# Optimization experiments

Measured on AMD Instinct MI355X. Metric: run time of the kernel, lower is better.

## Reference

```python
import jax, jax.numpy as jnp
import numpy as np
from jax import lax

B, T, S_ENC = 64, 32, 64
E, H, V = 1024, 1024, 32000


def setup_inputs() -> dict:
    key = jax.random.key(0)
    ks = jax.random.split(key, 12)
    s = 0.02
    return {
        "inputs": jax.random.randint(ks[0], (B, T), 0, V),
        "encoder_outputs": jax.random.normal(ks[1], (B, S_ENC, 2 * H), jnp.float32),
        "h0": jax.random.normal(ks[2], (B, H), jnp.float32) * 0.1,
        "c0": jax.random.normal(ks[3], (B, H), jnp.float32) * 0.1,
        "emb": jax.random.normal(ks[4], (V, E), jnp.float32) * s,
        "W_ih": jax.random.normal(ks[5], (4 * H, E), jnp.float32) * s,
        "W_hh": jax.random.normal(ks[6], (4 * H, H), jnp.float32) * s,
        "b_ih": jnp.zeros((4 * H,), jnp.float32),
        "b_hh": jnp.zeros((4 * H,), jnp.float32),
        "attn_W": jax.random.normal(ks[7], (2 * H, H), jnp.float32) * s,  # Linear(H -> 2H, no bias)
        "comb_W": jax.random.normal(ks[8], (H, 3 * H), jnp.float32) * s,  # Linear(3H -> H)
        "comb_b": jnp.zeros((H,), jnp.float32),
        "out_W": jax.random.normal(ks[9], (V, H), jnp.float32) * s,       # Linear(H -> V)
        "out_b": jnp.zeros((V,), jnp.float32),
    }


def _decode(inputs, encoder_outputs, h0, c0, emb, W_ih, W_hh, b_ih, b_hh,
            attn_W, comb_W, comb_b, out_W, out_b):
    x = emb[inputs]                      # [B, T, E]
    bias = b_ih + b_hh

    def step(carry, x_t):
        h, c = carry                     # [B, H] each
        gates = x_t @ W_ih.T + h @ W_hh.T + bias    # [B, 4H]
        i, f, g, o = jnp.split(gates, 4, axis=-1)   # PyTorch LSTM gate order
        i, f, o = jax.nn.sigmoid(i), jax.nn.sigmoid(f), jax.nn.sigmoid(o)
        c = f * c + i * jnp.tanh(g)
        h = o * jnp.tanh(c)
        # Luong-style attention (faithful to source, incl. softmax over dim=1 of size 1)
        ah = h @ attn_W.T                                        # [B, 2H]
        scores = jnp.einsum('bd,bsd->bs', ah, encoder_outputs)[:, None, :]  # [B,1,S]
        w = jax.nn.softmax(scores, axis=1)                       # size-1 axis -> all ones
        ctx = jnp.einsum('bqs,bsd->bqd', w, encoder_outputs)[:, 0]          # [B, 2H]
        merged = jnp.concatenate([h, ctx], axis=-1)              # [B, 3H]
        out = jnp.tanh(merged @ comb_W.T + comb_b)               # [B, H]
        return (h, c), out

    (h, c), outs = lax.scan(step, (h0, c0), x.transpose(1, 0, 2))
    outputs = outs.transpose(1, 0, 2)                            # [B, T, H]
    logits = outputs @ out_W.T + out_b                           # [B, T, V]
    return logits, h, c


def reference(inputs, encoder_outputs, h0, c0, emb, W_ih, W_hh, b_ih, b_hh,
              attn_W, comb_W, comb_b, out_W, out_b):
    return _decode(inputs, encoder_outputs, h0, c0, emb, W_ih, W_hh, b_ih, b_hh,
                   attn_W, comb_W, comb_b, out_W, out_b)
```

## Files before the change

kernel.cpp:

```cpp
#include <hip/hip_runtime.h>
#include <hip/hip_bf16.h>


typedef unsigned short u16;
typedef unsigned int u32;
typedef short s8v __attribute__((ext_vector_type(8)));
typedef float f4v __attribute__((ext_vector_type(4)));

__device__ __forceinline__ u16 f2bf(float f) {
  unsigned x = __float_as_uint(f);
  return (u16)((x + 0x7fffu + ((x >> 16) & 1u)) >> 16);
}
__device__ __forceinline__ float bf2f(u16 u) {
  return __uint_as_float(((unsigned)u) << 16);
}

__device__ __forceinline__ void gl_lds16(const void* g, void* l) {
  __builtin_amdgcn_global_load_lds(
      (const __attribute__((address_space(1))) u32*)g,
      (__attribute__((address_space(3))) u32*)l, 16, 0, 0);
}

__device__ __forceinline__ int xcd_swz(int bid, int nb) {
  int q8 = nb >> 3, r8 = nb & 7;
  int xcd = bid & 7, idx = bid >> 3;
  return (xcd < r8 ? xcd * (q8 + 1) : r8 * (q8 + 1) + (xcd - r8) * q8) + idx;
}

template <int EPI>
__global__ __launch_bounds__(512, 1) void gemm_q(
    const u16* __restrict__ A, const u16* __restrict__ Bm,
    const float* __restrict__ bias, void* __restrict__ Cp,
    int K, int ldc, int gridM) {
  __shared__ __align__(16) u16 LDS[2 * 32768];

  int swz = xcd_swz((int)blockIdx.x, (int)gridDim.x);
  int mt = swz % gridM, nt = swz / gridM;
  long bm = (long)mt * 256, bn = (long)nt * 256;

  int tid = threadIdx.x;
  int w = tid >> 6, l = tid & 63;
  int wm = w & 1, wn = w >> 1;
  int lr = l & 15, lg = l >> 4;

  int nt_k = K >> 6;

  auto stage = [&](int s, int kt_idx) {
    int kt = kt_idx << 6;
    u16* sa = &LDS[s * 32768];
    u16* sb = &LDS[s * 32768 + 16384];
#pragma unroll
    for (int ch = 0; ch < 4; ++ch) {
      int cb = ch * 512 + w * 64;
      int c = cb + l;
      int row = c >> 3, sp = c & 7;
      int ko = kt + ((sp ^ (row & 7)) << 3);
      gl_lds16(A + (bm + row) * (long)K + ko, sa + cb * 8);
      gl_lds16(Bm + (bn + row) * (long)K + ko, sb + cb * 8);
    }
  };

  f4v acc[8][4];
#pragma unroll
  for (int i = 0; i < 8; ++i)
#pragma unroll
    for (int j = 0; j < 4; ++j) acc[i][j] = (f4v){0.f, 0.f, 0.f, 0.f};

  stage(0, 0);
  asm volatile("s_waitcnt vmcnt(0)" ::: "memory");
  __builtin_amdgcn_s_barrier();
  __builtin_amdgcn_sched_barrier(0);

  for (int t = 0; t < nt_k; ++t) {
    if (t + 1 < nt_k) stage((t + 1) & 1, t + 1);
    const u16* sa = &LDS[(t & 1) * 32768];
    const u16* sb = &LDS[(t & 1) * 32768 + 16384];
#pragma unroll
    for (int ks = 0; ks < 2; ++ks) {
      s8v av[8], bv[4];
#pragma unroll
      for (int i = 0; i < 8; ++i) {
        int ra = wm * 128 + i * 16 + lr;
        int pa = (ks * 4 + lg) ^ (ra & 7);
        av[i] = *(const s8v*)((const char*)sa + ra * 128 + pa * 16);
      }
#pragma unroll
      for (int i = 0; i < 4; ++i) {
        int rb = wn * 64 + i * 16 + lr;
        int pb = (ks * 4 + lg) ^ (rb & 7);
        bv[i] = *(const s8v*)((const char*)sb + rb * 128 + pb * 16);
      }
      __builtin_amdgcn_s_setprio(1);
#pragma unroll
      for (int mi = 0; mi < 8; ++mi)
#pragma unroll
        for (int ni = 0; ni < 4; ++ni)
          acc[mi][ni] = __builtin_amdgcn_mfma_f32_16x16x32_bf16(
              av[mi], bv[ni], acc[mi][ni], 0, 0, 0);
      __builtin_amdgcn_s_setprio(0);
    }
    if (t + 1 >= nt_k) break;
    asm volatile("s_waitcnt vmcnt(0)" ::: "memory");
    __builtin_amdgcn_s_barrier();
    __builtin_amdgcn_sched_barrier(0);
  }

#pragma unroll
  for (int mi = 0; mi < 8; ++mi) {
#pragma unroll
    for (int q = 0; q < 4; ++q) {
      long row = bm + wm * 128 + mi * 16 + lg * 4 + q;
#pragma unroll
      for (int ni = 0; ni < 4; ++ni) {
        long col = bn + wn * 64 + ni * 16 + lr;
        float v = acc[mi][ni][q] + bias[col];
        if (EPI == 3)
          ((float*)Cp)[row * (long)ldc + col] = v;
        else
          ((u16*)Cp)[row * (long)ldc + col] = f2bf(v);
      }
    }
  }
}

template <int EPI, int PERM>
__global__ __launch_bounds__(512, 1) void gemm_p(
    const u16* __restrict__ A, const u16* __restrict__ Bm,
    const float* __restrict__ bias, void* __restrict__ Cp,
    int K, int ldc, int gridM) {
  __shared__ __align__(16) u16 LDS[3 * 24576];

  int swz = xcd_swz((int)blockIdx.x, (int)gridDim.x);
  int mt = swz % gridM, nt = swz / gridM;
  long bm = (long)mt * 128, bn = (long)nt * 256;

  int tid = threadIdx.x;
  int w = tid >> 6, l = tid & 63;
  int wm = w & 1, wn = w >> 1;
  int lr = l & 15, lg = l >> 4;

  int nt_k = K >> 6;

  auto stage = [&](int s, int kt_idx) {
    int kt = kt_idx << 6;
    u16* sa = &LDS[s * 24576];
    u16* sb = &LDS[s * 24576 + 8192];
#pragma unroll
    for (int ch = 0; ch < 2; ++ch) {
      int cb = ch * 512 + w * 64;
      int c = cb + l;
      int row = c >> 3, sp = c & 7;
      gl_lds16(A + (bm + row) * (long)K + kt + ((sp ^ (row & 7)) << 3),
               sa + cb * 8);
    }
#pragma unroll
    for (int ch = 0; ch < 4; ++ch) {
      int cb = ch * 512 + w * 64;
      int c = cb + l;
      int row = c >> 3, sp = c & 7;
      gl_lds16(Bm + (bn + row) * (long)K + kt + ((sp ^ (row & 7)) << 3),
               sb + cb * 8);
    }
  };

  f4v acc[4][4];
#pragma unroll
  for (int i = 0; i < 4; ++i)
#pragma unroll
    for (int j = 0; j < 4; ++j) acc[i][j] = (f4v){0.f, 0.f, 0.f, 0.f};

  stage(0, 0);
  stage(1, 1);
  asm volatile("s_waitcnt vmcnt(6)" ::: "memory");
  __builtin_amdgcn_s_barrier();
  __builtin_amdgcn_sched_barrier(0);

  for (int t = 0; t < nt_k; ++t) {
    if (t + 2 < nt_k) stage((t + 2) % 3, t + 2);
    const u16* sa = &LDS[(t % 3) * 24576];
    const u16* sb = &LDS[(t % 3) * 24576 + 8192];
#pragma unroll
    for (int ks = 0; ks < 2; ++ks) {
      s8v av[4], bv[4];
#pragma unroll
      for (int i = 0; i < 4; ++i) {
        int ra = wm * 64 + i * 16 + lr;
        int pa = (ks * 4 + lg) ^ (ra & 7);
        av[i] = *(const s8v*)((const char*)sa + ra * 128 + pa * 16);
        int rb = wn * 64 + i * 16 + lr;
        int pb = (ks * 4 + lg) ^ (rb & 7);
        bv[i] = *(const s8v*)((const char*)sb + rb * 128 + pb * 16);
      }
      __builtin_amdgcn_s_setprio(1);
#pragma unroll
      for (int mi = 0; mi < 4; ++mi)
#pragma unroll
        for (int ni = 0; ni < 4; ++ni)
          acc[mi][ni] = __builtin_amdgcn_mfma_f32_16x16x32_bf16(
              av[mi], bv[ni], acc[mi][ni], 0, 0, 0);
      __builtin_amdgcn_s_setprio(0);
    }
    if (t + 1 >= nt_k) break;
    if (t + 2 < nt_k) {
      asm volatile("s_waitcnt vmcnt(6)" ::: "memory");
    } else {
      asm volatile("s_waitcnt vmcnt(0)" ::: "memory");
    }
    __builtin_amdgcn_s_barrier();
    __builtin_amdgcn_sched_barrier(0);
  }

#pragma unroll
  for (int mi = 0; mi < 4; ++mi) {
#pragma unroll
    for (int q = 0; q < 4; ++q) {
      long row = bm + wm * 64 + mi * 16 + lg * 4 + q;
#pragma unroll
      for (int ni = 0; ni < 4; ++ni) {
        long col = bn + wn * 64 + ni * 16 + lr;
        float v = acc[mi][ni][q] + bias[col];
        if (PERM) {
          long prow = (row & 31) * 64 + (row >> 5);
          long pcol = (col & 1023) * 4 + (col >> 10);
          ((u16*)Cp)[prow * 4096 + pcol] = f2bf(v);
        } else if (EPI == 3) {
          ((float*)Cp)[row * (long)ldc + col] = v;
        } else {
          ((u16*)Cp)[row * (long)ldc + col] = f2bf(v);
        }
      }
    }
  }
}

template <int EPI>
__global__ __launch_bounds__(256, 2) void gemm_bt2(
    const u16* __restrict__ A, const u16* __restrict__ Bm,
    const float* __restrict__ bias, void* __restrict__ Cp,
    int K, int ldc, int gridM) {
  __shared__ __align__(16) u16 As[128 * 64];
  __shared__ __align__(16) u16 Bs[128 * 64];

  int swz = xcd_swz((int)blockIdx.x, (int)gridDim.x);
  int mt = swz % gridM, nt = swz / gridM;
  long bm = (long)mt * 128, bn = (long)nt * 128;

  int tid = threadIdx.x;
  int w = tid >> 6, l = tid & 63;
  int wm = (w & 1) * 64, wn = (w >> 1) * 64;
  int lr = l & 15, lg = l >> 4;

  f4v acc[4][4];
#pragma unroll
  for (int i = 0; i < 4; ++i)
#pragma unroll
    for (int j = 0; j < 4; ++j) acc[i][j] = (f4v){0.f, 0.f, 0.f, 0.f};

  for (int kt = 0; kt < K; kt += 64) {
#pragma unroll
    for (int p = 0; p < 4; ++p) {
      int cb = (p * 4 + w) * 64;
      int c = cb + l;
      int row = c >> 3, ce = (c & 7) * 8;
      gl_lds16(A + (bm + row) * (long)K + kt + ce, &As[cb * 8]);
      gl_lds16(Bm + (bn + row) * (long)K + kt + ce, &Bs[cb * 8]);
    }
    __syncthreads();
#pragma unroll
    for (int ks = 0; ks < 2; ++ks) {
      int kb = ks * 64 + lg * 16;
      s8v av[4], bv[4];
#pragma unroll
      for (int i = 0; i < 4; ++i) {
        av[i] = *(const s8v*)((const char*)&As[0] + (wm + i * 16 + lr) * 128 + kb);
        bv[i] = *(const s8v*)((const char*)&Bs[0] + (wn + i * 16 + lr) * 128 + kb);
      }
#pragma unroll
      for (int mi = 0; mi < 4; ++mi)
#pragma unroll
        for (int ni = 0; ni < 4; ++ni)
          acc[mi][ni] = __builtin_amdgcn_mfma_f32_16x16x32_bf16(
              av[mi], bv[ni], acc[mi][ni], 0, 0, 0);
    }
    __syncthreads();
  }
#pragma unroll
  for (int mi = 0; mi < 4; ++mi) {
#pragma unroll
    for (int q = 0; q < 4; ++q) {
      long row = bm + wm + mi * 16 + lg * 4 + q;
#pragma unroll
      for (int ni = 0; ni < 4; ++ni) {
        long col = bn + wn + ni * 16 + lr;
        float v = acc[mi][ni][q] + bias[col];
        if (EPI == 2) v = tanhf(v);
        if (EPI == 3)
          ((float*)Cp)[row * (long)ldc + col] = v;
        else
          ((u16*)Cp)[row * (long)ldc + col] = f2bf(v);
      }
    }
  }
}

template <int EPI, int PERM>
__global__ __launch_bounds__(256, 2) void gemm_btf(
    const u16* __restrict__ A, const float* __restrict__ Bm,
    const float* __restrict__ bias, void* __restrict__ Cp,
    int K, int ldc, int gridM) {
  __shared__ __align__(16) u16 As[128][72];
  __shared__ __align__(16) u16 Bs[128][72];
  int swz = xcd_swz((int)blockIdx.x, (int)gridDim.x);
  int mt = swz % gridM, nt = swz / gridM;
  long bm = (long)mt * 128, bn = (long)nt * 128;
  int tid = threadIdx.x;
  int w = tid >> 6, l = tid & 63;
  int wm = (w & 1) * 64, wn = (w >> 1) * 64;
  int lr = l & 15, lg = l >> 4;
  f4v acc[4][4];
#pragma unroll
  for (int i = 0; i < 4; ++i)
#pragma unroll
    for (int j = 0; j < 4; ++j) acc[i][j] = (f4v){0.f, 0.f, 0.f, 0.f};
  for (int kt = 0; kt < K; kt += 64) {
#pragma unroll
    for (int p = 0; p < 4; ++p) {
      int ch = p * 256 + tid;
      int row = ch >> 3, cc = ch & 7;
      *(uint4*)((char*)(&As[0][0]) + row * 144 + cc * 16) =
          *(const uint4*)(A + (bm + row) * (long)K + kt + cc * 8);
      const float* bp = Bm + (bn + row) * (long)K + kt + cc * 8;
      float4 b0 = *(const float4*)bp;
      float4 b1 = *(const float4*)(bp + 4);
      union { u16 t8[8]; uint4 v; } cv;
      cv.t8[0] = f2bf(b0.x); cv.t8[1] = f2bf(b0.y);
      cv.t8[2] = f2bf(b0.z); cv.t8[3] = f2bf(b0.w);
      cv.t8[4] = f2bf(b1.x); cv.t8[5] = f2bf(b1.y);
      cv.t8[6] = f2bf(b1.z); cv.t8[7] = f2bf(b1.w);
      *(uint4*)((char*)(&Bs[0][0]) + row * 144 + cc * 16) = cv.v;
    }
    __syncthreads();
#pragma unroll
    for (int ks = 0; ks < 2; ++ks) {
      int kb = ks * 64 + lg * 16;
      s8v av[4], bv[4];
#pragma unroll
      for (int i = 0; i < 4; ++i) {
        av[i] = *(const s8v*)((const char*)(&As[0][0]) + (wm + i * 16 + lr) * 144 + kb);
        bv[i] = *(const s8v*)((const char*)(&Bs[0][0]) + (wn + i * 16 + lr) * 144 + kb);
      }
#pragma unroll
      for (int mi = 0; mi < 4; ++mi)
#pragma unroll
        for (int ni = 0; ni < 4; ++ni)
          acc[mi][ni] = __builtin_amdgcn_mfma_f32_16x16x32_bf16(
              av[mi], bv[ni], acc[mi][ni], 0, 0, 0);
    }
    __syncthreads();
  }
#pragma unroll
  for (int mi = 0; mi < 4; ++mi) {
#pragma unroll
    for (int q = 0; q < 4; ++q) {
      long row = bm + wm + mi * 16 + lg * 4 + q;
#pragma unroll
      for (int ni = 0; ni < 4; ++ni) {
        long col = bn + wn + ni * 16 + lr;
        float v = acc[mi][ni][q] + bias[col];
        if (EPI == 2) v = tanhf(v);
        if (PERM) {
          long prow = (row & 31) * 64 + (row >> 5);
          long pcol = (col & 1023) * 4 + (col >> 10);
          ((u16*)Cp)[prow * 4096 + pcol] = f2bf(v);
        } else if (EPI == 3) {
          ((float*)Cp)[row * (long)ldc + col] = v;
        } else {
          ((u16*)Cp)[row * (long)ldc + col] = f2bf(v);
        }
      }
    }
  }
}

__global__ __launch_bounds__(256, 1) void lstm_step3(
    const u16* __restrict__ Whh, const u16* __restrict__ xprojT,
    const u16* __restrict__ h_in, u16* __restrict__ h_next,
    float* __restrict__ c_buf, u16* __restrict__ a2,
    float* __restrict__ hf, float* __restrict__ cf, int t) {
  __shared__ __align__(16) u16 Hs[32 * 1024];
  __shared__ __align__(16) u16 Ws[32 * 1024];
  __shared__ float Gs[32][33];

  int bid = blockIdx.x;
  int j = bid & 127, bh = bid >> 7;
  int colbase = j * 8;
  int tid = threadIdx.x, w = tid >> 6, l = tid & 63;
  int bq = w & 1, nh = w >> 1;
  int lr = l & 15, lg = l >> 4;

  int hi = tid >> 7;
  int ps = tid & 127;
#pragma unroll
  for (int p = 0; p < 16; ++p) {
    int r = 2 * p + hi;
    int sl = ps ^ (r & 7);
    gl_lds16(h_in + (bh * 32 + r) * 1024 + sl * 8, &Hs[(p * 4 + w) * 512]);
    int g = r >> 3, rr = r & 7;
    gl_lds16(Whh + (long)(g * 1024 + colbase + rr) * 1024 + sl * 8,
             &Ws[(p * 4 + w) * 512]);
  }

  int eb = tid >> 3, er = tid & 7;
  int gb = bh * 32 + eb, ecol = colbase + er;
  uint2 xv = *(const uint2*)(xprojT + ((long)t * 64 + gb) * 4096 + ecol * 4);
  float co = c_buf[gb * 1024 + ecol];
  __syncthreads();

  int ar = bq * 16 + lr;
  int br = nh * 16 + lr;
  int axor = (ar & 7), bxor = (br & 7);
  f4v acc0 = {0.f, 0.f, 0.f, 0.f}, acc1 = {0.f, 0.f, 0.f, 0.f};
#pragma unroll
  for (int kc = 0; kc < 32; kc += 2) {
    {
      int s = kc * 4 + lg;
      s8v av = *(const s8v*)((const char*)Hs + ar * 2048 + (s ^ axor) * 16);
      s8v bv = *(const s8v*)((const char*)Ws + br * 2048 + (s ^ bxor) * 16);
      acc0 = __builtin_amdgcn_mfma_f32_16x16x32_bf16(av, bv, acc0, 0, 0, 0);
    }
    {
      int s = (kc + 1) * 4 + lg;
      s8v av = *(const s8v*)((const char*)Hs + ar * 2048 + (s ^ axor) * 16);
      s8v bv = *(const s8v*)((const char*)Ws + br * 2048 + (s ^ bxor) * 16);
      acc1 = __builtin_amdgcn_mfma_f32_16x16x32_bf16(av, bv, acc1, 0, 0, 0);
    }
  }
#pragma unroll
  for (int q = 0; q < 4; ++q)
    Gs[bq * 16 + lg * 4 + q][nh * 16 + lr] = acc0[q] + acc1[q];
  __syncthreads();

  float pi = Gs[eb][er]      + bf2f((u16)(xv.x));
  float pf = Gs[eb][8 + er]  + bf2f((u16)(xv.x >> 16));
  float pg = Gs[eb][16 + er] + bf2f((u16)(xv.y));
  float po = Gs[eb][24 + er] + bf2f((u16)(xv.y >> 16));
  float iv = 1.f / (1.f + expf(-pi));
  float fv = 1.f / (1.f + expf(-pf));
  float ov = 1.f / (1.f + expf(-po));
  float gv = tanhf(pg);
  float cn = fv * co + iv * gv;
  float hn = ov * tanhf(cn);
  c_buf[gb * 1024 + ecol] = cn;
  u16 hb = f2bf(hn);
  h_next[gb * 1024 + ecol] = hb;
  a2[(long)(gb * 32 + t) * 3072 + ecol] = hb;
  if (t == 31) {
    hf[gb * 1024 + ecol] = hn;
    cf[gb * 1024 + ecol] = cn;
  }
}

__global__ void k_misc(const float* __restrict__ bih, const float* __restrict__ bhh,
                       const float* __restrict__ h0, const float* __restrict__ c0,
                       float* __restrict__ bias, u16* __restrict__ hbuf0,
                       float* __restrict__ cbuf) {
  int i = blockIdx.x * 256 + threadIdx.x;
  if (i < 4096) bias[i] = bih[i] + bhh[i];
  if (i < 65536) {
    hbuf0[i] = f2bf(h0[i]);
    cbuf[i] = c0[i];
  }
}

__global__ void k_cvt8(const float* __restrict__ src, u16* __restrict__ dst, int n8) {
  int i = blockIdx.x * 256 + threadIdx.x;
  if (i >= n8) return;
  const float4* s = (const float4*)(src + (long)i * 8);
  float4 a = s[0], b = s[1];
  union { u16 t[8]; uint4 v; } cv;
  cv.t[0] = f2bf(a.x); cv.t[1] = f2bf(a.y); cv.t[2] = f2bf(a.z); cv.t[3] = f2bf(a.w);
  cv.t[4] = f2bf(b.x); cv.t[5] = f2bf(b.y); cv.t[6] = f2bf(b.z); cv.t[7] = f2bf(b.w);
  ((uint4*)dst)[i] = cv.v;
}

__global__ void k_emb8(const int* __restrict__ inp, const float* __restrict__ emb,
                       u16* __restrict__ dst) {
  int i = blockIdx.x * 256 + threadIdx.x;
  int r = i >> 7, k8 = (i & 127) * 8;
  const float* s = emb + (long)inp[r] * 1024 + k8;
  float4 a = *(const float4*)s, b = *(const float4*)(s + 4);
  union { u16 t[8]; uint4 v; } cv;
  cv.t[0] = f2bf(a.x); cv.t[1] = f2bf(a.y); cv.t[2] = f2bf(a.z); cv.t[3] = f2bf(a.w);
  cv.t[4] = f2bf(b.x); cv.t[5] = f2bf(b.y); cv.t[6] = f2bf(b.z); cv.t[7] = f2bf(b.w);
  ((uint4*)dst)[i] = cv.v;
}

__global__ void k_ctx2(const float* __restrict__ enc, u16* __restrict__ a2) {
  int b = blockIdx.x;
  int dg = threadIdx.x;
  float s[8] = {0.f, 0.f, 0.f, 0.f, 0.f, 0.f, 0.f, 0.f};
  for (int si = 0; si < 64; ++si) {
    const float* p = enc + ((long)(b * 64 + si)) * 2048 + dg * 8;
    float4 x = *(const float4*)p, y = *(const float4*)(p + 4);
    s[0] += x.x; s[1] += x.y; s[2] += x.z; s[3] += x.w;
    s[4] += y.x; s[5] += y.y; s[6] += y.z; s[7] += y.w;
  }
  union { u16 t[8]; uint4 v; } cv;
#pragma unroll
  for (int e = 0; e < 8; ++e) cv.t[e] = f2bf(s[e]);
  for (int t = 0; t < 32; ++t)
    *(uint4*)(a2 + (long)(b * 32 + t) * 3072 + 1024 + dg * 8) = cv.v;
}

extern "C" void kernel_launch(void* const* d_in, const int* in_sizes, int n_in,
                              void* d_out, int out_size, void* d_ws, size_t ws_size,
                              hipStream_t stream) {
  (void)in_sizes; (void)n_in; (void)out_size;
  const int*   inputs = (const int*)d_in[0];
  const float* enc    = (const float*)d_in[1];
  const float* h0     = (const float*)d_in[2];
  const float* c0     = (const float*)d_in[3];
  const float* emb    = (const float*)d_in[4];
  const float* Wih    = (const float*)d_in[5];
  const float* Whh    = (const float*)d_in[6];
  const float* bih    = (const float*)d_in[7];
  const float* bhh    = (const float*)d_in[8];
  const float* combW  = (const float*)d_in[10];
  const float* combb  = (const float*)d_in[11];
  const float* outW   = (const float*)d_in[12];
  const float* outb   = (const float*)d_in[13];
  float* out = (float*)d_out;

  char* ws = (char*)d_ws;
  size_t off = 0;
  auto alloc = [&](size_t bytes) {
    char* p = ws + off;
    off += (bytes + 255) & ~(size_t)255;
    return p;
  };
  u16*   WHH_BF = (u16*)  alloc(4096ull * 1024 * 2);
  u16*   XPROJ  = (u16*)  alloc(2048ull * 4096 * 2);
  u16*   EMBX   = (u16*)  alloc(2048ull * 1024 * 2);
  u16*   A2     = (u16*)  alloc(2048ull * 3072 * 2);
  u16*   OUTS   = (u16*)  alloc(2048ull * 1024 * 2);
  float* BIAS   = (float*)alloc(4096 * 4);
  u16*   HBUF   = (u16*)  alloc(2ull * 65536 * 2);
  float* CBUF   = (float*)alloc(65536 * 4);
  u16*   WIH_BF   = (u16*)alloc(4096ull * 1024 * 2);
  u16*   COMBW_BF = (u16*)alloc(1024ull * 3072 * 2);
  size_t off_w1 = off;
  u16*   OUTW_BF  = (u16*)alloc(32000ull * 1024 * 2);
  size_t off_w2 = off;
  bool haveW1 = ws_size >= off_w1;
  bool haveW2 = ws_size >= off_w2;

  k_misc<<<dim3(256), dim3(256), 0, stream>>>(bih, bhh, h0, c0, BIAS, HBUF, CBUF);
  k_cvt8<<<dim3(2048), dim3(256), 0, stream>>>(Whh, WHH_BF, 524288);
  k_emb8<<<dim3(1024), dim3(256), 0, stream>>>(inputs, emb, EMBX);
  k_ctx2<<<dim3(64), dim3(256), 0, stream>>>(enc, A2);
  if (haveW1) {
    k_cvt8<<<dim3(2048), dim3(256), 0, stream>>>(Wih, WIH_BF, 524288);
    k_cvt8<<<dim3(1536), dim3(256), 0, stream>>>(combW, COMBW_BF, 393216);
  }
  if (haveW2)
    k_cvt8<<<dim3(16000), dim3(256), 0, stream>>>(outW, OUTW_BF, 4096000);

  if (haveW1)
    gemm_p<1, 1><<<dim3(256), dim3(512), 0, stream>>>(EMBX, WIH_BF, BIAS, XPROJ,
                                                      1024, 4096, 16);
  else
    gemm_btf<1, 1><<<dim3(512), dim3(256), 0, stream>>>(EMBX, Wih, BIAS, XPROJ,
                                                        1024, 4096, 16);

  for (int t = 0; t < 32; ++t) {
    u16* hin  = HBUF + (t & 1) * 65536;
    u16* hout = HBUF + ((t + 1) & 1) * 65536;
    lstm_step3<<<dim3(256), dim3(256), 0, stream>>>(
        WHH_BF, XPROJ, hin, hout, CBUF, A2,
        out + 65536000, out + 65536000 + 65536, t);
  }

  if (haveW1)
    gemm_bt2<2><<<dim3(128), dim3(256), 0, stream>>>(A2, COMBW_BF, combb, OUTS,
                                                     3072, 1024, 16);
  else
    gemm_btf<2, 0><<<dim3(128), dim3(256), 0, stream>>>(A2, combW, combb, OUTS,
                                                        3072, 1024, 16);
  if (haveW2)
    gemm_q<3><<<dim3(1000), dim3(512), 0, stream>>>(OUTS, OUTW_BF, outb, d_out,
                                                    1024, 32000, 8);
  else
    gemm_btf<3, 0><<<dim3(4000), dim3(256), 0, stream>>>(OUTS, outW, outb, d_out,
                                                         1024, 32000, 16);
}
```

Before: 558.4 us.

## Split output GEMM k-loop into four barrier-synced phases with interleaved half-tile staging

Restructures the vocab-projection GEMM main loop into four sub-phases, each doing its LDS fragment reads and then a half of the MFMA work, with barriers between phases. Prefetch of the next K tile is split into per-operand, per-half loads issued inside the first two phases, so global-to-LDS traffic overlaps with compute rather than being issued in one burst. The aim is better overlap of memory and matrix-core work in the largest GEMM. In exchange it adds more barriers per iteration. Waves 0 and 2 wait only with vmcnt(4), so they leave their last loads outstanding across the barrier, which risks reading second-half data that has not yet landed.

```diff
diff --git a/kernel.cpp b/kernel.cpp
--- a/kernel.cpp
+++ b/kernel.cpp
@@ -28,7 +28,7 @@
 }
 
 template <int EPI>
-__global__ __launch_bounds__(512, 1) void gemm_q(
+__global__ __launch_bounds__(512, 1) void gemm_8p(
     const u16* __restrict__ A, const u16* __restrict__ Bm,
     const float* __restrict__ bias, void* __restrict__ Cp,
     int K, int ldc, int gridM) {
@@ -45,18 +45,19 @@
 
   int nt_k = K >> 6;
 
-  auto stage = [&](int s, int kt_idx) {
+  auto stage_unit = [&](int s, int kt_idx, int op, int h) {
     int kt = kt_idx << 6;
-    u16* sa = &LDS[s * 32768];
-    u16* sb = &LDS[s * 32768 + 16384];
-#pragma unroll
-    for (int ch = 0; ch < 4; ++ch) {
-      int cb = ch * 512 + w * 64;
+    const u16* src = op ? Bm : A;
+    long base = op ? bn : bm;
+    u16* dst = &LDS[s * 32768 + op * 16384 + h * 8192];
+#pragma unroll
+    for (int p = 0; p < 2; ++p) {
+      int cb = p * 512 + w * 64;
       int c = cb + l;
-      int row = c >> 3, sp = c & 7;
-      int ko = kt + ((sp ^ (row & 7)) << 3);
-      gl_lds16(A + (bm + row) * (long)K + ko, sa + cb * 8);
-      gl_lds16(Bm + (bn + row) * (long)K + ko, sb + cb * 8);
+      int row = h * 128 + (c >> 3);
+      int sp = c & 7;
+      int sl = sp ^ (row & 7);
+      gl_lds16(src + (base + row) * (long)K + kt + sl * 8, dst + cb * 8);
     }
   };
 
@@ -66,44 +67,71 @@
 #pragma unroll
     for (int j = 0; j < 4; ++j) acc[i][j] = (f4v){0.f, 0.f, 0.f, 0.f};
 
-  stage(0, 0);
+  stage_unit(0, 0, 0, 0); stage_unit(0, 0, 1, 0);
+  stage_unit(0, 0, 0, 1); stage_unit(0, 0, 1, 1);
   asm volatile("s_waitcnt vmcnt(0)" ::: "memory");
   __builtin_amdgcn_s_barrier();
   __builtin_amdgcn_sched_barrier(0);
 
+  bool fastw = (w == 0) || (w == 2);
+
+#define GP_PHASE(ks, nh, dostage, h)                                         \
+  {                                                                          \
+    s8v av[8], bv[2];                                                        \
+    _Pragma("unroll")                                                        \
+    for (int mi = 0; mi < 8; ++mi) {                                         \
+      int ra = wm * 128 + mi * 16 + lr;                                      \
+      int sp = ((ks) * 4 + lg) ^ (ra & 7);                                   \
+      av[mi] = *(const s8v*)(&LDS[cur * 32768 + ra * 64 + sp * 8]);          \
+    }                                                                        \
+    _Pragma("unroll")                                                        \
+    for (int nj = 0; nj < 2; ++nj) {                                         \
+      int rb = wn * 64 + ((nh) * 2 + nj) * 16 + lr;                          \
+      int sp = ((ks) * 4 + lg) ^ (rb & 7);                                   \
+      bv[nj] = *(const s8v*)(&LDS[cur * 32768 + 16384 + rb * 64 + sp * 8]);  \
+    }                                                                        \
+    if (dostage) {                                                           \
+      stage_unit(nxt, t + 1, 0, (h));                                        \
+      stage_unit(nxt, t + 1, 1, (h));                                        \
+    }                                                                        \
+    __builtin_amdgcn_sched_barrier(0);                                       \
+    __builtin_amdgcn_s_barrier();                                            \
+    __builtin_amdgcn_sched_barrier(0);                                       \
+    __builtin_amdgcn_s_setprio(1);                                           \
+    _Pragma("unroll")                                                        \
+    for (int mi = 0; mi < 8; ++mi) {                                         \
+      acc[mi][(nh) * 2] = __builtin_amdgcn_mfma_f32_16x16x32_bf16(           \
+          av[mi], bv[0], acc[mi][(nh) * 2], 0, 0, 0);                        \
+      acc[mi][(nh) * 2 + 1] = __builtin_amdgcn_mfma_f32_16x16x32_bf16(       \
+          av[mi], bv[1], acc[mi][(nh) * 2 + 1], 0, 0, 0);                    \
+    }                                                                        \
+    __builtin_amdgcn_s_setprio(0);                                           \
+  }
+
   for (int t = 0; t < nt_k; ++t) {
-    if (t + 1 < nt_k) stage((t + 1) & 1, t + 1);
-    const u16* sa = &LDS[(t & 1) * 32768];
-    const u16* sb = &LDS[(t & 1) * 32768 + 16384];
-#pragma unroll
-    for (int ks = 0; ks < 2; ++ks) {
-      s8v av[8], bv[4];
-#pragma unroll
-      for (int i = 0; i < 8; ++i) {
-        int ra = wm * 128 + i * 16 + lr;
-        int pa = (ks * 4 + lg) ^ (ra & 7);
-        av[i] = *(const s8v*)((const char*)sa + ra * 128 + pa * 16);
-      }
-#pragma unroll
-      for (int i = 0; i < 4; ++i) {
-        int rb = wn * 64 + i * 16 + lr;
-        int pb = (ks * 4 + lg) ^ (rb & 7);
-        bv[i] = *(const s8v*)((const char*)sb + rb * 128 + pb * 16);
-      }
-      __builtin_amdgcn_s_setprio(1);
-#pragma unroll
-      for (int mi = 0; mi < 8; ++mi)
-#pragma unroll
-        for (int ni = 0; ni < 4; ++ni)
-          acc[mi][ni] = __builtin_amdgcn_mfma_f32_16x16x32_bf16(
-              av[mi], bv[ni], acc[mi][ni], 0, 0, 0);
-      __builtin_amdgcn_s_setprio(0);
-    }
-    if (t + 1 >= nt_k) break;
-    asm volatile("s_waitcnt vmcnt(0)" ::: "memory");
+    int cur = t & 1, nxt = cur ^ 1;
+    bool st = (t + 1 < nt_k);
+    GP_PHASE(0, 0, st, 0)
+    __builtin_amdgcn_sched_barrier(0);
     __builtin_amdgcn_s_barrier();
+    GP_PHASE(0, 1, st, 1)
     __builtin_amdgcn_sched_barrier(0);
-  }
+    __builtin_amdgcn_s_barrier();
+    GP_PHASE(1, 0, false, 0)
+    __builtin_amdgcn_sched_barrier(0);
+    __builtin_amdgcn_s_barrier();
+    GP_PHASE(1, 1, false, 0)
+    if (st) {
+      if (fastw) {
+        asm volatile("s_waitcnt vmcnt(4)" ::: "memory");
+      } else {
+        asm volatile("s_waitcnt vmcnt(0)" ::: "memory");
+      }
+    }
+    __builtin_amdgcn_sched_barrier(0);
+    __builtin_amdgcn_s_barrier();
+  }
+#undef GP_PHASE
 
 #pragma unroll
   for (int mi = 0; mi < 8; ++mi) {
@@ -587,8 +615,8 @@
     gemm_btf<2, 0><<<dim3(128), dim3(256), 0, stream>>>(A2, combW, combb, OUTS,
                                                         3072, 1024, 16);
   if (haveW2)
-    gemm_q<3><<<dim3(1000), dim3(512), 0, stream>>>(OUTS, OUTW_BF, outb, d_out,
-                                                    1024, 32000, 8);
+    gemm_8p<3><<<dim3(1000), dim3(512), 0, stream>>>(OUTS, OUTW_BF, outb, d_out,
+                                                     1024, 32000, 8);
   else
     gemm_btf<3, 0><<<dim3(4000), dim3(256), 0, stream>>>(OUTS, outW, outb, d_out,
                                                          1024, 32000, 16);
```

Result: no change. 569.1 us (+1.9%).
